# Kernel optimization log

Measured on AMD Instinct MI355X. Metric: run time of the kernel, lower is better.

## Reference

```python
import jax, jax.numpy as jnp
import numpy as np

TOP_K = 2

def setup_inputs() -> dict:
    key = jax.random.key(0)
    k0, k1, k2, k3 = jax.random.split(key, 4)
    B, T, D, F, E = 2, 2048, 1024, 4096, 8
    x = jax.random.normal(k0, (B, T, D), dtype=jnp.float32)
    Wr = jax.random.normal(k1, (E, D), dtype=jnp.float32) * 0.02   # router weight [out=E, in=D]
    W1 = jax.random.normal(k2, (E, F, D), dtype=jnp.float32) * 0.02  # per-expert up-proj [out=F, in=D]
    W2 = jax.random.normal(k3, (E, D, F), dtype=jnp.float32) * 0.02  # per-expert down-proj [out=D, in=F]
    return {"x": x, "Wr": Wr, "W1": W1, "W2": W2}

def reference(x, Wr, W1, W2):
    B, T, D = x.shape
    E = Wr.shape[0]
    N = B * T
    xf = x.reshape(N, D)
    # Router in fp32 on the un-cast activations (as in the torch module).
    logits = xf @ Wr.T                                   # [N, E]
    probs = jax.nn.softmax(logits, axis=-1)
    topk_w, topk_idx = jax.lax.top_k(probs, TOP_K)       # [N, K]
    topk_w = topk_w / jnp.sum(topk_w, axis=-1, keepdims=True)
    # Combine weights scattered into a dense [N, E] dispatch/combine matrix
    # (top_k indices are distinct, so .set is exact).
    combine = jnp.zeros((N, E), dtype=jnp.float32)
    combine = combine.at[jnp.arange(N)[:, None], topk_idx].set(topk_w)
    # Expert FFN runs in bf16 (comm_dtype in the original all-to-all pipeline).
    xb = xf.astype(jnp.bfloat16)
    h = jax.nn.gelu(jnp.einsum('nd,efd->enf', xb, W1.astype(jnp.bfloat16)),
                    approximate=False)                   # [E, N, F]
    yo = jnp.einsum('enf,edf->end', h, W2.astype(jnp.bfloat16))  # [E, N, D]
    # Weighted combine: bf16 expert outputs * fp32 gate weights -> fp32 (torch promotion).
    out = jnp.einsum('end,ne->nd', yo.astype(jnp.float32), combine)
    return out.reshape(B, T, D)
```

## Files before the change

kernel.cpp:

```cpp
#include <hip/hip_runtime.h>
#include <hip/hip_bf16.h>

typedef __attribute__((ext_vector_type(8))) __bf16 bf16x8;
typedef __attribute__((ext_vector_type(4))) float floatx4;

constexpr int N_TOK = 4096;
constexpr int DDIM  = 1024;
constexpr int FDIM  = 4096;
constexpr int NEXP  = 8;
constexpr int NSLOT = 2 * N_TOK;
constexpr int MAXT  = 72;
constexpr int KSPLIT = 2;
constexpr int NN_UP = FDIM / 128;
constexpr int NN_DN = DDIM / 128;

static __device__ __forceinline__ unsigned short f2bf(float f) {
    union { __hip_bfloat16 h; unsigned short u; } v;
    v.h = __float2bfloat16(f);
    return v.u;
}

static __device__ __forceinline__ void gl2lds16(const unsigned short* g, unsigned short* l) {
    __builtin_amdgcn_global_load_lds(
        (__attribute__((address_space(1))) void*)g,
        (__attribute__((address_space(3))) void*)l,
        16, 0, 0);
}

__global__ void castW_kernel(const float* __restrict__ W1, const float* __restrict__ W2,
                             unsigned short* __restrict__ w1b, unsigned short* __restrict__ w2b,
                             int* __restrict__ counts) {
    constexpr int HALF = NEXP * FDIM * DDIM / 4;
    int i = blockIdx.x * 256 + threadIdx.x;
    const float* s; unsigned short* d; int j;
    if (i < HALF) { s = W1; d = w1b; j = i; }
    else          { s = W2; d = w2b; j = i - HALF; }
    float4 v = *(const float4*)(s + (size_t)j * 4);
    ushort4 o;
    o.x = f2bf(v.x); o.y = f2bf(v.y); o.z = f2bf(v.z); o.w = f2bf(v.w);
    *(ushort4*)(d + (size_t)j * 4) = o;
    if (blockIdx.x == 0 && threadIdx.x < NEXP) counts[threadIdx.x] = 0;
}

__global__ void router_kernel(const float* __restrict__ x, const float* __restrict__ Wr,
                              unsigned short* __restrict__ xb,
                              int* __restrict__ te, float* __restrict__ tw,
                              int* __restrict__ counts) {
    __shared__ float wr[NEXP * DDIM];
    const int tid = threadIdx.x;
    for (int i = tid; i < NEXP * DDIM; i += 256) wr[i] = Wr[i];
    __syncthreads();
    const int wave = tid >> 6, lane = tid & 63;
    const int t = blockIdx.x * 4 + wave;

    float xr[16];
    const float* xp = x + (size_t)t * DDIM;
    #pragma unroll
    for (int i = 0; i < 16; i++) xr[i] = xp[lane + 64 * i];

    unsigned short* xbp = xb + (size_t)t * DDIM;
    #pragma unroll
    for (int i = 0; i < 16; i++) xbp[lane + 64 * i] = f2bf(xr[i]);

    float logit[NEXP];
    #pragma unroll
    for (int e = 0; e < NEXP; e++) {
        float s = 0.f;
        #pragma unroll
        for (int i = 0; i < 16; i++) s += xr[i] * wr[e * DDIM + lane + 64 * i];
        #pragma unroll
        for (int off = 32; off > 0; off >>= 1) s += __shfl_xor(s, off, 64);
        logit[e] = s;
    }
    if (lane == 0) {
        int i0 = 0; float l0 = logit[0];
        #pragma unroll
        for (int e = 1; e < NEXP; e++) if (logit[e] > l0) { l0 = logit[e]; i0 = e; }
        int i1 = -1; float l1 = -3.0e38f;
        #pragma unroll
        for (int e = 0; e < NEXP; e++) if (e != i0 && logit[e] > l1) { l1 = logit[e]; i1 = e; }
        float p1 = expf(l1 - l0);
        float w0 = 1.f / (1.f + p1);
        float w1 = p1 * w0;
        te[t * 2] = i0; te[t * 2 + 1] = i1;
        tw[t * 2] = w0; tw[t * 2 + 1] = w1;
        atomicAdd(&counts[i0], 1);
        atomicAdd(&counts[i1], 1);
    }
}

__global__ void scan_scatter_kernel(const int* __restrict__ counts,
                                    const int* __restrict__ te, const float* __restrict__ tw,
                                    int* __restrict__ offsets, int* __restrict__ tile_em,
                                    int* __restrict__ ntile,
                                    int* __restrict__ rowid, float* __restrict__ gate,
                                    int* __restrict__ tok2slot) {
    __shared__ int soff[NEXP];
    __shared__ int scur[NEXP];
    const int tid = threadIdx.x;
    if (tid == 0) {
        int acc = 0, nt = 0;
        for (int e = 0; e < NEXP; e++) {
            offsets[e] = acc; soff[e] = acc;
            for (int m0 = 0; m0 < counts[e]; m0 += 128)
                tile_em[nt++] = (e << 16) | (m0 >> 7);
            acc += counts[e];
        }
        offsets[NEXP] = acc;
        ntile[0] = nt;
        for (int i = nt; i < MAXT; i++) tile_em[i] = 0;
    }
    if (tid < NEXP) scur[tid] = 0;
    __syncthreads();
    for (int t = tid; t < N_TOK; t += 256) {
        #pragma unroll
        for (int k = 0; k < 2; k++) {
            int e = te[t * 2 + k];
            int pos = atomicAdd(&scur[e], 1);
            int slot = soff[e] + pos;
            rowid[slot] = t;
            gate[slot] = tw[t * 2 + k];
            tok2slot[t * 2 + k] = slot;
        }
    }
}

template <bool UP>
__global__ __launch_bounds__(256)
void ffn_gemm(const unsigned short* __restrict__ A,
              const unsigned short* __restrict__ Wb,
              unsigned short* __restrict__ Hout,
              float* __restrict__ Y,
              const int* __restrict__ rowid,
              const float* __restrict__ gate,
              const int* __restrict__ offsets,
              const int* __restrict__ tile_em,
              const int* __restrict__ ntile) {
    constexpr int BM = 128, BN = 128, BK = 32, LDT = 32;
    constexpr int NOUT = UP ? FDIM : DDIM;
    constexpr int KDIM = UP ? DDIM : FDIM;
    constexpr int NN   = UP ? NN_UP : NN_DN;
    constexpr int KLEN = UP ? DDIM : (FDIM / KSPLIT);

    const int id = blockIdx.x;
    const int n0 = (id % NN) * BN;
    const int bt = (id / NN) % MAXT;
    const int ks = UP ? 0 : (id / (NN * MAXT));
    if (bt >= ntile[0]) return;
    const int em = tile_em[bt];
    const int e  = em >> 16;
    const int m0 = (em & 0xffff) << 7;
    const int seg = offsets[e];
    const int cnt = offsets[e + 1] - seg;
    const int kbase = ks * KLEN;

    __shared__ __align__(16) unsigned short As[BM * LDT];
    __shared__ __align__(16) unsigned short Bs[BN * LDT];

    const int tid  = threadIdx.x;
    const int lane = tid & 63;
    const int wave = tid >> 6;

    const int srow0 = wave * 32 + (lane >> 2);
    const int chunk = lane & 3;

    const unsigned short* ag[2];
    #pragma unroll
    for (int j = 0; j < 2; j++) {
        int r = srow0 + j * 16;
        int slot = seg + m0 + r;
        if (slot >= NSLOT) slot = NSLOT - 1;
        if (UP) { int t = rowid[slot]; ag[j] = A + (size_t)t * DDIM + kbase + chunk * 8; }
        else    { ag[j] = A + (size_t)slot * FDIM + kbase + chunk * 8; }
    }
    const unsigned short* bg[2];
    #pragma unroll
    for (int j = 0; j < 2; j++) {
        int r = srow0 + j * 16;
        bg[j] = Wb + ((size_t)e * NOUT + n0 + r) * KDIM + kbase + chunk * 8;
    }
    unsigned short* asl[2];
    unsigned short* bsl[2];
    #pragma unroll
    for (int j = 0; j < 2; j++) {
        asl[j] = &As[(wave * 32 + j * 16) * LDT] + lane * 8;
        bsl[j] = &Bs[(wave * 32 + j * 16) * LDT] + lane * 8;
    }

    const int wm = (wave >> 1) * 64;
    const int wn = (wave & 1) * 64;
    const int frow = lane & 15;
    const int quad = lane >> 4;

    floatx4 acc[4][4];
    #pragma unroll
    for (int i = 0; i < 4; i++)
        #pragma unroll
        for (int j = 0; j < 4; j++)
            acc[i][j] = (floatx4){0.f, 0.f, 0.f, 0.f};

    for (int k0 = 0; k0 < KLEN; k0 += BK) {
        __syncthreads();
        gl2lds16(ag[0], asl[0]);
        gl2lds16(ag[1], asl[1]);
        gl2lds16(bg[0], bsl[0]);
        gl2lds16(bg[1], bsl[1]);
        ag[0] += BK; ag[1] += BK; bg[0] += BK; bg[1] += BK;
        __syncthreads();

        bf16x8 av[4], bv[4];
        #pragma unroll
        for (int i = 0; i < 4; i++)
            av[i] = *(const bf16x8*)&As[(wm + i * 16 + frow) * LDT + quad * 8];
        #pragma unroll
        for (int i = 0; i < 4; i++)
            bv[i] = *(const bf16x8*)&Bs[(wn + i * 16 + frow) * LDT + quad * 8];
        #pragma unroll
        for (int mt = 0; mt < 4; mt++)
            #pragma unroll
            for (int nt = 0; nt < 4; nt++)
                acc[mt][nt] = __builtin_amdgcn_mfma_f32_16x16x32_bf16(av[mt], bv[nt], acc[mt][nt], 0, 0, 0);
    }

    #pragma unroll
    for (int mt = 0; mt < 4; mt++) {
        #pragma unroll
        for (int r = 0; r < 4; r++) {
            int mloc = m0 + wm + mt * 16 + quad * 4 + r;
            if (mloc >= cnt) continue;
            int slot = seg + mloc;
            if (UP) {
                #pragma unroll
                for (int nt = 0; nt < 4; nt++) {
                    int n = n0 + wn + nt * 16 + frow;
                    float v = acc[mt][nt][r];
                    float g = 0.5f * v * (1.0f + erff(v * 0.70710678118654752f));
                    Hout[(size_t)slot * FDIM + n] = f2bf(g);
                }
            } else {
                float gw = gate[slot];
                #pragma unroll
                for (int nt = 0; nt < 4; nt++) {
                    int n = n0 + wn + nt * 16 + frow;
                    Y[((size_t)ks * NSLOT + slot) * DDIM + n] = gw * acc[mt][nt][r];
                }
            }
        }
    }
}

__global__ void combine_kernel(const float* __restrict__ Y, const int* __restrict__ tok2slot,
                               float* __restrict__ out) {
    int idx = blockIdx.x * 256 + threadIdx.x;
    int t = idx >> 8;
    int c = (idx & 255) * 4;
    int s0 = tok2slot[t * 2], s1 = tok2slot[t * 2 + 1];
    float4 r = make_float4(0.f, 0.f, 0.f, 0.f);
    #pragma unroll
    for (int ks = 0; ks < KSPLIT; ks++) {
        float4 a = *(const float4*)(Y + ((size_t)ks * NSLOT + s0) * DDIM + c);
        float4 b = *(const float4*)(Y + ((size_t)ks * NSLOT + s1) * DDIM + c);
        r.x += a.x + b.x; r.y += a.y + b.y; r.z += a.z + b.z; r.w += a.w + b.w;
    }
    *(float4*)(out + (size_t)t * DDIM + c) = r;
}

extern "C" void kernel_launch(void* const* d_in, const int* in_sizes, int n_in,
                              void* d_out, int out_size, void* d_ws, size_t ws_size,
                              hipStream_t stream) {
    const float* x  = (const float*)d_in[0];
    const float* Wr = (const float*)d_in[1];
    const float* W1 = (const float*)d_in[2];
    const float* W2 = (const float*)d_in[3];
    float* out = (float*)d_out;

    char* ws = (char*)d_ws;
    size_t off = 0;
    auto alloc = [&](size_t bytes) -> char* {
        char* p = ws + off;
        off = (off + bytes + 255) & ~(size_t)255;
        return p;
    };
    unsigned short* xb   = (unsigned short*)alloc((size_t)N_TOK * DDIM * 2);
    unsigned short* H    = (unsigned short*)alloc((size_t)NSLOT * FDIM * 2);
    float* Yb      = (float*)alloc((size_t)KSPLIT * NSLOT * DDIM * 4);
    int*   rowid   = (int*)alloc(NSLOT * 4);
    float* gatew   = (float*)alloc(NSLOT * 4);
    int*   te      = (int*)alloc(NSLOT * 4);
    float* tw      = (float*)alloc(NSLOT * 4);
    int*   t2s     = (int*)alloc(NSLOT * 4);
    int*   counts  = (int*)alloc(64);
    int*   offsets = (int*)alloc(64);
    int*   tile_em = (int*)alloc(MAXT * 4);
    int*   ntile   = (int*)alloc(64);
    unsigned short* w1b = (unsigned short*)alloc((size_t)NEXP * FDIM * DDIM * 2);
    unsigned short* w2b = (unsigned short*)alloc((size_t)NEXP * DDIM * FDIM * 2);
    (void)ws_size;

    castW_kernel<<<2 * NEXP * FDIM * DDIM / 4 / 256, 256, 0, stream>>>(W1, W2, w1b, w2b, counts);
    router_kernel<<<N_TOK / 4, 256, 0, stream>>>(x, Wr, xb, te, tw, counts);
    scan_scatter_kernel<<<1, 256, 0, stream>>>(counts, te, tw, offsets, tile_em, ntile,
                                               rowid, gatew, t2s);
    ffn_gemm<true ><<<NN_UP * MAXT, 256, 0, stream>>>(xb, w1b, H, Yb, rowid, gatew,
                                                      offsets, tile_em, ntile);
    ffn_gemm<false><<<NN_DN * MAXT * KSPLIT, 256, 0, stream>>>(H, w2b, H, Yb, rowid, gatew,
                                                               offsets, tile_em, ntile);
    combine_kernel<<<N_TOK, 256, 0, stream>>>(Yb, t2s, out);
}
```

Before: 669.8 us.

## Enlarge MoE GEMM tiles, double-buffer LDS, swizzle layout, remap blocks per XCD

The grouped expert GEMMs now use 256-row token tiles, 256- or 128-column output tiles and BK=64 with 512-thread blocks. The LDS tiles are double-buffered so the next K-slice loads while MFMAs run, and the LDS columns are XOR-swizzled to avoid bank conflicts. Block IDs are remapped so consecutive logical tiles land on the same XCD for L2 reuse. Larger tiles raise arithmetic intensity and cut barriers, at the cost of more padding waste per expert, fewer workgroups and higher register/LDS pressure.

```diff
diff --git a/kernel.cpp b/kernel.cpp
--- a/kernel.cpp
+++ b/kernel.cpp
@@ -9,10 +9,9 @@
 constexpr int FDIM  = 4096;
 constexpr int NEXP  = 8;
 constexpr int NSLOT = 2 * N_TOK;
-constexpr int MAXT  = 72;
+constexpr int BM_T  = 256;
+constexpr int MAXT  = NSLOT / BM_T + NEXP - 1;
 constexpr int KSPLIT = 2;
-constexpr int NN_UP = FDIM / 128;
-constexpr int NN_DN = DDIM / 128;
 
 static __device__ __forceinline__ unsigned short f2bf(float f) {
     union { __hip_bfloat16 h; unsigned short u; } v;
@@ -102,8 +101,8 @@
         int acc = 0, nt = 0;
         for (int e = 0; e < NEXP; e++) {
             offsets[e] = acc; soff[e] = acc;
-            for (int m0 = 0; m0 < counts[e]; m0 += 128)
-                tile_em[nt++] = (e << 16) | (m0 >> 7);
+            for (int m0 = 0; m0 < counts[e]; m0 += BM_T)
+                tile_em[nt++] = (e << 16) | (m0 >> 8);
             acc += counts[e];
         }
         offsets[NEXP] = acc;
@@ -126,7 +125,7 @@
 }
 
 template <bool UP>
-__global__ __launch_bounds__(256)
+__global__ __launch_bounds__(512)
 void ffn_gemm(const unsigned short* __restrict__ A,
               const unsigned short* __restrict__ Wb,
               unsigned short* __restrict__ Hout,
@@ -136,113 +135,138 @@
               const int* __restrict__ offsets,
               const int* __restrict__ tile_em,
               const int* __restrict__ ntile) {
-    constexpr int BM = 128, BN = 128, BK = 32, LDT = 32;
+    constexpr int BM = 256;
+    constexpr int BN = UP ? 256 : 128;
+    constexpr int BK = 64;
     constexpr int NOUT = UP ? FDIM : DDIM;
     constexpr int KDIM = UP ? DDIM : FDIM;
-    constexpr int NN   = UP ? NN_UP : NN_DN;
+    constexpr int NN   = NOUT / BN;
     constexpr int KLEN = UP ? DDIM : (FDIM / KSPLIT);
-
-    const int id = blockIdx.x;
+    constexpr int KT   = KLEN / BK;
+    constexpr int WN_W = UP ? 4 : 2;
+    constexpr int MREP = UP ? 8 : 4;
+    constexpr int NREP = 4;
+    constexpr int AINST = BM / 64;
+    constexpr int BINST = BN / 64;
+    constexpr int ASTRIDE = BM * BK;
+    constexpr int BSTRIDE = BN * BK;
+
+    const int nwg = NN * MAXT * (UP ? 1 : KSPLIT);
+    const int orig = blockIdx.x;
+    const int xcd = orig & 7, idx = orig >> 3;
+    const int q = nwg >> 3, r = nwg & 7;
+    const int id = (xcd < r ? xcd * (q + 1) : r * (q + 1) + (xcd - r) * q) + idx;
+
     const int n0 = (id % NN) * BN;
     const int bt = (id / NN) % MAXT;
     const int ks = UP ? 0 : (id / (NN * MAXT));
     if (bt >= ntile[0]) return;
     const int em = tile_em[bt];
     const int e  = em >> 16;
-    const int m0 = (em & 0xffff) << 7;
+    const int m0 = (em & 0xffff) << 8;
     const int seg = offsets[e];
     const int cnt = offsets[e + 1] - seg;
     const int kbase = ks * KLEN;
 
-    __shared__ __align__(16) unsigned short As[BM * LDT];
-    __shared__ __align__(16) unsigned short Bs[BN * LDT];
+    __shared__ __align__(16) unsigned short As[2 * ASTRIDE];
+    __shared__ __align__(16) unsigned short Bs[2 * BSTRIDE];
 
     const int tid  = threadIdx.x;
     const int lane = tid & 63;
     const int wave = tid >> 6;
-
-    const int srow0 = wave * 32 + (lane >> 2);
-    const int chunk = lane & 3;
-
-    const unsigned short* ag[2];
-    #pragma unroll
-    for (int j = 0; j < 2; j++) {
-        int r = srow0 + j * 16;
-        int slot = seg + m0 + r;
+    const int lrow = lane >> 3;
+    const int scol = ((lane & 7) ^ lrow) * 8;
+
+    const unsigned short* ag[AINST];
+    #pragma unroll
+    for (int j = 0; j < AINST; j++) {
+        int arow = wave * (BM / 8) + j * 8 + lrow;
+        int slot = seg + m0 + arow;
         if (slot >= NSLOT) slot = NSLOT - 1;
-        if (UP) { int t = rowid[slot]; ag[j] = A + (size_t)t * DDIM + kbase + chunk * 8; }
-        else    { ag[j] = A + (size_t)slot * FDIM + kbase + chunk * 8; }
-    }
-    const unsigned short* bg[2];
-    #pragma unroll
-    for (int j = 0; j < 2; j++) {
-        int r = srow0 + j * 16;
-        bg[j] = Wb + ((size_t)e * NOUT + n0 + r) * KDIM + kbase + chunk * 8;
-    }
-    unsigned short* asl[2];
-    unsigned short* bsl[2];
-    #pragma unroll
-    for (int j = 0; j < 2; j++) {
-        asl[j] = &As[(wave * 32 + j * 16) * LDT] + lane * 8;
-        bsl[j] = &Bs[(wave * 32 + j * 16) * LDT] + lane * 8;
-    }
-
-    const int wm = (wave >> 1) * 64;
-    const int wn = (wave & 1) * 64;
+        if (UP) { int t = rowid[slot]; ag[j] = A + (size_t)t * DDIM + kbase + scol; }
+        else    { ag[j] = A + (size_t)slot * FDIM + kbase + scol; }
+    }
+    const unsigned short* bg[BINST];
+    #pragma unroll
+    for (int j = 0; j < BINST; j++) {
+        int brow = wave * (BN / 8) + j * 8 + lrow;
+        bg[j] = Wb + ((size_t)e * NOUT + n0 + brow) * KDIM + kbase + scol;
+    }
+    unsigned short* asl[AINST];
+    unsigned short* bsl[BINST];
+    #pragma unroll
+    for (int j = 0; j < AINST; j++)
+        asl[j] = &As[(wave * (BM / 8) + j * 8) * BK] + lane * 8;
+    #pragma unroll
+    for (int j = 0; j < BINST; j++)
+        bsl[j] = &Bs[(wave * (BN / 8) + j * 8) * BK] + lane * 8;
+
+    auto stage = [&](int b) {
+        #pragma unroll
+        for (int j = 0; j < AINST; j++) { gl2lds16(ag[j], asl[j] + b * ASTRIDE); ag[j] += BK; }
+        #pragma unroll
+        for (int j = 0; j < BINST; j++) { gl2lds16(bg[j], bsl[j] + b * BSTRIDE); bg[j] += BK; }
+    };
+
     const int frow = lane & 15;
     const int quad = lane >> 4;
-
-    floatx4 acc[4][4];
-    #pragma unroll
-    for (int i = 0; i < 4; i++)
-        #pragma unroll
-        for (int j = 0; j < 4; j++)
+    const int wm = (wave / WN_W) * (MREP * 16);
+    const int wn = (wave % WN_W) * 64;
+    const int sxor = (frow & 7) << 3;
+
+    floatx4 acc[MREP][NREP];
+    #pragma unroll
+    for (int i = 0; i < MREP; i++)
+        #pragma unroll
+        for (int j = 0; j < NREP; j++)
             acc[i][j] = (floatx4){0.f, 0.f, 0.f, 0.f};
 
-    for (int k0 = 0; k0 < KLEN; k0 += BK) {
+    stage(0);
+    __syncthreads();
+    for (int kt = 0; kt < KT; kt++) {
+        if (kt + 1 < KT) stage((kt + 1) & 1);
+        const unsigned short* Ab = &As[(kt & 1) * ASTRIDE];
+        const unsigned short* Bb = &Bs[(kt & 1) * BSTRIDE];
+        #pragma unroll
+        for (int h = 0; h < 2; h++) {
+            const int cs = (h * 32 + quad * 8) ^ sxor;
+            bf16x8 av[MREP], bv[NREP];
+            #pragma unroll
+            for (int i = 0; i < MREP; i++)
+                av[i] = *(const bf16x8*)&Ab[(wm + i * 16 + frow) * BK + cs];
+            #pragma unroll
+            for (int j = 0; j < NREP; j++)
+                bv[j] = *(const bf16x8*)&Bb[(wn + j * 16 + frow) * BK + cs];
+            #pragma unroll
+            for (int i = 0; i < MREP; i++)
+                #pragma unroll
+                for (int j = 0; j < NREP; j++)
+                    acc[i][j] = __builtin_amdgcn_mfma_f32_16x16x32_bf16(av[i], bv[j], acc[i][j], 0, 0, 0);
+        }
         __syncthreads();
-        gl2lds16(ag[0], asl[0]);
-        gl2lds16(ag[1], asl[1]);
-        gl2lds16(bg[0], bsl[0]);
-        gl2lds16(bg[1], bsl[1]);
-        ag[0] += BK; ag[1] += BK; bg[0] += BK; bg[1] += BK;
-        __syncthreads();
-
-        bf16x8 av[4], bv[4];
-        #pragma unroll
-        for (int i = 0; i < 4; i++)
-            av[i] = *(const bf16x8*)&As[(wm + i * 16 + frow) * LDT + quad * 8];
-        #pragma unroll
-        for (int i = 0; i < 4; i++)
-            bv[i] = *(const bf16x8*)&Bs[(wn + i * 16 + frow) * LDT + quad * 8];
-        #pragma unroll
-        for (int mt = 0; mt < 4; mt++)
-            #pragma unroll
-            for (int nt = 0; nt < 4; nt++)
-                acc[mt][nt] = __builtin_amdgcn_mfma_f32_16x16x32_bf16(av[mt], bv[nt], acc[mt][nt], 0, 0, 0);
-    }
-
-    #pragma unroll
-    for (int mt = 0; mt < 4; mt++) {
-        #pragma unroll
-        for (int r = 0; r < 4; r++) {
-            int mloc = m0 + wm + mt * 16 + quad * 4 + r;
+    }
+
+    #pragma unroll
+    for (int mt = 0; mt < MREP; mt++) {
+        #pragma unroll
+        for (int rr = 0; rr < 4; rr++) {
+            int mloc = m0 + wm + mt * 16 + quad * 4 + rr;
             if (mloc >= cnt) continue;
             int slot = seg + mloc;
             if (UP) {
                 #pragma unroll
-                for (int nt = 0; nt < 4; nt++) {
+                for (int nt = 0; nt < NREP; nt++) {
                     int n = n0 + wn + nt * 16 + frow;
-                    float v = acc[mt][nt][r];
+                    float v = acc[mt][nt][rr];
                     float g = 0.5f * v * (1.0f + erff(v * 0.70710678118654752f));
                     Hout[(size_t)slot * FDIM + n] = f2bf(g);
                 }
             } else {
                 float gw = gate[slot];
                 #pragma unroll
-                for (int nt = 0; nt < 4; nt++) {
+                for (int nt = 0; nt < NREP; nt++) {
                     int n = n0 + wn + nt * 16 + frow;
-                    Y[((size_t)ks * NSLOT + slot) * DDIM + n] = gw * acc[mt][nt][r];
+                    Y[((size_t)ks * NSLOT + slot) * DDIM + n] = gw * acc[mt][nt][rr];
                 }
             }
         }
@@ -297,13 +321,16 @@
     unsigned short* w2b = (unsigned short*)alloc((size_t)NEXP * DDIM * FDIM * 2);
     (void)ws_size;
 
+    constexpr int GRID_UP = (FDIM / 256) * MAXT;
+    constexpr int GRID_DN = (DDIM / 128) * MAXT * KSPLIT;
+
     castW_kernel<<<2 * NEXP * FDIM * DDIM / 4 / 256, 256, 0, stream>>>(W1, W2, w1b, w2b, counts);
     router_kernel<<<N_TOK / 4, 256, 0, stream>>>(x, Wr, xb, te, tw, counts);
     scan_scatter_kernel<<<1, 256, 0, stream>>>(counts, te, tw, offsets, tile_em, ntile,
                                                rowid, gatew, t2s);
-    ffn_gemm<true ><<<NN_UP * MAXT, 256, 0, stream>>>(xb, w1b, H, Yb, rowid, gatew,
-                                                      offsets, tile_em, ntile);
-    ffn_gemm<false><<<NN_DN * MAXT * KSPLIT, 256, 0, stream>>>(H, w2b, H, Yb, rowid, gatew,
-                                                               offsets, tile_em, ntile);
+    ffn_gemm<true ><<<GRID_UP, 512, 0, stream>>>(xb, w1b, H, Yb, rowid, gatew,
+                                                 offsets, tile_em, ntile);
+    ffn_gemm<false><<<GRID_DN, 512, 0, stream>>>(H, w2b, H, Yb, rowid, gatew,
+                                                 offsets, tile_em, ntile);
     combine_kernel<<<N_TOK, 256, 0, stream>>>(Yb, t2s, out);
 }
```

Measured after the change: 762.2 us. +13.8%, slower.
